# Optimization experiments

Measured on AMD Instinct MI355X. Metric: run time of the kernel, lower is better.

## Reference

```python
import jax, jax.numpy as jnp
import numpy as np

N, T, E = 50000, 8, 800000
X_DIM, H_DIM, Z_DIM = 128, 64, 32


def setup_inputs() -> dict:
    key = jax.random.key(0)
    k = jax.random.split(key, 6)
    x = jax.random.normal(k[0], (N, X_DIM), dtype=jnp.float32)
    ei = jax.random.randint(k[1], (T, 2, E), 0, N, dtype=jnp.int32)
    ew = jax.random.uniform(k[2], (T, E), dtype=jnp.float32)
    W1 = jax.random.normal(k[3], (X_DIM, H_DIM), dtype=jnp.float32) * 0.1
    b1 = jnp.zeros((H_DIM,), dtype=jnp.float32)
    W2 = jax.random.normal(k[4], (H_DIM, Z_DIM), dtype=jnp.float32) * 0.1
    b2 = jnp.zeros((Z_DIM,), dtype=jnp.float32)
    return {"x": x, "ei": ei, "ew": ew, "W1": W1, "b1": b1, "W2": W2, "b2": b2}


def gcn_layer(x, src, dst, ew, W, b):
    # PyG GCNConv with add_self_loops=True (self-loop weight 1):
    #   out = D^{-1/2} (A + I) D^{-1/2} (x @ W) + b,  deg from edge weights at dst
    n = x.shape[0]
    loop = jnp.arange(n, dtype=src.dtype)
    s = jnp.concatenate([src, loop])            # [E+N]
    d = jnp.concatenate([dst, loop])            # [E+N]
    w = jnp.concatenate([ew, jnp.ones((n,), ew.dtype)])
    deg = jax.ops.segment_sum(w, d, num_segments=n)      # [N]
    dinv = jnp.where(deg > 0, jax.lax.rsqrt(deg), 0.0)
    norm = dinv[s] * w * dinv[d]                # [E+N]
    h = x @ W                                    # [N, out_dim] linear first
    out = jax.ops.segment_sum(h[s] * norm[:, None], d, num_segments=n)
    return out + b


def reference(x, ei, ew, W1, b1, W2, b2):
    # eval mode: Dropout(0.25) and DropEdge(0.5) are identity (inner_forward calls self.eval())
    def step(carry, inputs):
        ei_t, ew_t = inputs
        src, dst = ei_t[0], ei_t[1]
        h = jax.nn.relu(gcn_layer(x, src, dst, ew_t, W1, b1))
        z = jnp.tanh(gcn_layer(h, src, dst, ew_t, W2, b2))
        return carry, z
    _, zs = jax.lax.scan(step, None, (ei, ew))   # [T, N, Z_DIM]
    return zs
```

## Files before the change

kernel.cpp:

```cpp
#include <hip/hip_runtime.h>
#include <hip/hip_fp16.h>
#include <math.h>

#define N_NODES 50000
#define T_STEPS 8
#define E_EDGES 800000
#define XD 128
#define HD 64
#define ZD 32
#define M_TOT (T_STEPS * N_NODES)
#define TE_TOT (T_STEPS * E_EDGES)

#define NBKT 196
#define BPT 125
#define EPB 6400
#define NBLK_A (T_STEPS * BPT)
#define CNTA_LEN (T_STEPS * NBKT * BPT)
#define NBUCK_T (T_STEPS * NBKT)
#define BKT_CAP 4864

#define SCAN_CH 2048
#define SCANA_NB ((CNTA_LEN + SCAN_CH - 1) / SCAN_CH)

__device__ __forceinline__ float4 h4tof4(ushort4 u) {
  return make_float4(__half2float(__ushort_as_half(u.x)),
                     __half2float(__ushort_as_half(u.y)),
                     __half2float(__ushort_as_half(u.z)),
                     __half2float(__ushort_as_half(u.w)));
}
__device__ __forceinline__ float cnorm(unsigned int c) {
  return __half2float(__ushort_as_half((unsigned short)(c >> 16)));
}

__global__ __launch_bounds__(256) void k_h0(const float* __restrict__ x,
                                            const float* __restrict__ W1,
                                            unsigned short* __restrict__ h0h) {
  __shared__ float xs[256 * 33];
  __shared__ float w1s[32 * 64];
  const int tid = threadIdx.x;
  const int nb = blockIdx.x * 256;
  const int nl_base = tid & 63;
  const int jg = tid >> 6;
  const float4* x4 = (const float4*)x;
  const float4* W14 = (const float4*)W1;

  float acc[4][16];
#pragma unroll
  for (int i = 0; i < 4; ++i)
#pragma unroll
    for (int j = 0; j < 16; ++j) acc[i][j] = 0.f;

  for (int kc = 0; kc < 4; ++kc) {
#pragma unroll
    for (int r = 0; r < 8; ++r) {
      int f4 = tid + r * 256;
      int nl = f4 >> 3;
      int k4 = f4 & 7;
      float4 v = make_float4(0.f, 0.f, 0.f, 0.f);
      int node = nb + nl;
      if (node < N_NODES) v = x4[node * 32 + kc * 8 + k4];
      int base = nl * 33 + k4 * 4;
      xs[base + 0] = v.x; xs[base + 1] = v.y;
      xs[base + 2] = v.z; xs[base + 3] = v.w;
    }
#pragma unroll
    for (int r = 0; r < 2; ++r) {
      int f4 = tid + r * 256;
      ((float4*)w1s)[f4] = W14[kc * 512 + f4];
    }
    __syncthreads();
#pragma unroll 4
    for (int k = 0; k < 32; ++k) {
      float xv[4];
#pragma unroll
      for (int i = 0; i < 4; ++i) xv[i] = xs[(nl_base + i * 64) * 33 + k];
      const float* wr = &w1s[k * 64 + jg * 16];
      float4 w0 = *(const float4*)(wr + 0);
      float4 w1v = *(const float4*)(wr + 4);
      float4 w2v = *(const float4*)(wr + 8);
      float4 w3v = *(const float4*)(wr + 12);
#pragma unroll
      for (int i = 0; i < 4; ++i) {
        acc[i][0] += xv[i] * w0.x;  acc[i][1] += xv[i] * w0.y;
        acc[i][2] += xv[i] * w0.z;  acc[i][3] += xv[i] * w0.w;
        acc[i][4] += xv[i] * w1v.x; acc[i][5] += xv[i] * w1v.y;
        acc[i][6] += xv[i] * w1v.z; acc[i][7] += xv[i] * w1v.w;
        acc[i][8] += xv[i] * w2v.x; acc[i][9] += xv[i] * w2v.y;
        acc[i][10] += xv[i] * w2v.z; acc[i][11] += xv[i] * w2v.w;
        acc[i][12] += xv[i] * w3v.x; acc[i][13] += xv[i] * w3v.y;
        acc[i][14] += xv[i] * w3v.z; acc[i][15] += xv[i] * w3v.w;
      }
    }
    __syncthreads();
  }
  ushort4* h4p = (ushort4*)h0h;
#pragma unroll
  for (int i = 0; i < 4; ++i) {
    int node = nb + nl_base + i * 64;
    if (node < N_NODES) {
#pragma unroll
      for (int q = 0; q < 4; ++q) {
        ushort4 s;
        s.x = __half_as_ushort(__float2half(acc[i][q * 4 + 0]));
        s.y = __half_as_ushort(__float2half(acc[i][q * 4 + 1]));
        s.z = __half_as_ushort(__float2half(acc[i][q * 4 + 2]));
        s.w = __half_as_ushort(__float2half(acc[i][q * 4 + 3]));
        h4p[(size_t)node * 16 + jg * 4 + q] = s;
      }
    }
  }
}

__global__ __launch_bounds__(256) void k_binhist(const int* __restrict__ ei,
                                                 unsigned short* __restrict__ rankA,
                                                 unsigned int* __restrict__ cntA) {
  __shared__ unsigned int hist[NBKT];
  const int tid = threadIdx.x, bid = blockIdx.x;
  const int t = bid / BPT, b = bid - t * BPT;
  if (tid < NBKT) hist[tid] = 0;
  __syncthreads();
  const int* dstp = ei + (t * 2 + 1) * E_EDGES + b * EPB;
  const int gbase = t * E_EDGES + b * EPB;
#pragma unroll
  for (int it = 0; it < EPB / 256; ++it) {
    int e = it * 256 + tid;
    int dst = dstp[e];
    unsigned int r = atomicAdd(&hist[dst >> 8], 1u);
    rankA[gbase + e] = (unsigned short)r;
  }
  __syncthreads();
  if (tid < NBKT) cntA[(t * NBKT + tid) * BPT + b] = hist[tid];
}

__global__ __launch_bounds__(256) void k_scan1(const unsigned int* __restrict__ cntA,
                                               int* __restrict__ bsum) {
  __shared__ int s[256];
  int bid = blockIdx.x, tid = threadIdx.x;
  int base = bid * SCAN_CH;
  int v = 0;
#pragma unroll
  for (int r = 0; r < 8; ++r) {
    int i = base + tid + r * 256;
    if (i < CNTA_LEN) v += (int)cntA[i];
  }
  s[tid] = v;
  __syncthreads();
  for (int off = 128; off > 0; off >>= 1) {
    if (tid < off) s[tid] += s[tid + off];
    __syncthreads();
  }
  if (tid == 0) bsum[bid] = s[0];
}

__global__ __launch_bounds__(256) void k_scan2(const int* __restrict__ bsum,
                                               int* __restrict__ bpre) {
  __shared__ int s[256];
  int tid = threadIdx.x;
  int v = (tid < SCANA_NB) ? bsum[tid] : 0;
  s[tid] = v;
  __syncthreads();
  for (int off = 1; off < 256; off <<= 1) {
    int t = (tid >= off) ? s[tid - off] : 0;
    __syncthreads();
    s[tid] += t;
    __syncthreads();
  }
  bpre[tid] = s[tid] - v;
}

__global__ __launch_bounds__(256) void k_scan3(const unsigned int* __restrict__ cntA,
                                               const int* __restrict__ bpre,
                                               unsigned int* __restrict__ scannedA) {
  __shared__ int s[256];
  int bid = blockIdx.x, tid = threadIdx.x;
  int i0 = bid * SCAN_CH + tid * 8;
  int c[8];
  int lsum = 0;
#pragma unroll
  for (int j = 0; j < 8; ++j) {
    int i = i0 + j;
    c[j] = (i < CNTA_LEN) ? (int)cntA[i] : 0;
    lsum += c[j];
  }
  int v = lsum;
  s[tid] = v;
  __syncthreads();
  for (int off = 1; off < 256; off <<= 1) {
    int t = (tid >= off) ? s[tid - off] : 0;
    __syncthreads();
    s[tid] += t;
    __syncthreads();
  }
  int run = bpre[bid] + (s[tid] - v);
#pragma unroll
  for (int j = 0; j < 8; ++j) {
    int i = i0 + j;
    if (i < CNTA_LEN) {
      scannedA[i] = (unsigned int)run;
      run += c[j];
    }
  }
}

__global__ __launch_bounds__(256) void k_binscatter(const int* __restrict__ ei,
                                                    const float* __restrict__ ew,
                                                    const unsigned short* __restrict__ rankA,
                                                    const unsigned int* __restrict__ scannedA,
                                                    uint2* __restrict__ ebuf) {
  int i = blockIdx.x * 256 + threadIdx.x;
  int t = i / E_EDGES;
  int e = i - t * E_EDGES;
  int b = e / EPB;
  int src = ei[t * 2 * E_EDGES + e];
  int dst = ei[(t * 2 + 1) * E_EDGES + e];
  float w = ew[i];
  int bkt = dst >> 8;
  unsigned int pos = scannedA[(t * NBKT + bkt) * BPT + b] + rankA[i];
  ebuf[pos] = make_uint2(((unsigned int)(dst & 255) << 16) | (unsigned int)src,
                         __float_as_uint(w));
}

__global__ __launch_bounds__(256) void k_bucket1(const uint2* __restrict__ ebuf,
                                                 const unsigned int* __restrict__ scannedA,
                                                 unsigned int* __restrict__ localscan,
                                                 float* __restrict__ dinv,
                                                 int* __restrict__ row_off) {
  __shared__ unsigned int cnt[256];
  __shared__ float degs[256];
  __shared__ unsigned int sc[256];
  const int tid = threadIdx.x, blk = blockIdx.x;
  const int t = blk / NBKT, bkt = blk - t * NBKT;
  const unsigned int base = scannedA[blk * BPT];
  const unsigned int end = (blk == NBUCK_T - 1) ? (unsigned int)TE_TOT
                                                : scannedA[(blk + 1) * BPT];
  cnt[tid] = 0;
  degs[tid] = 0.f;
  __syncthreads();
  for (unsigned int i = base + tid; i < end; i += 256) {
    uint2 v = ebuf[i];
    unsigned int dlo = v.x >> 16;
    atomicAdd(&cnt[dlo], 1u);
    atomicAdd(&degs[dlo], __uint_as_float(v.y));
  }
  __syncthreads();
  unsigned int myc = cnt[tid];
  sc[tid] = myc;
  __syncthreads();
  for (int off = 1; off < 256; off <<= 1) {
    unsigned int a = (tid >= off) ? sc[tid - off] : 0;
    __syncthreads();
    sc[tid] += a;
    __syncthreads();
  }
  unsigned int start = base + (sc[tid] - myc);
  localscan[blk * 256 + tid] = start;
  int dst = bkt * 256 + tid;
  if (dst < N_NODES) {
    int tn = t * N_NODES + dst;
    dinv[tn] = rsqrtf(1.0f + degs[tid]);
    row_off[tn] = (int)start;
  }
  if (blk == NBUCK_T - 1 && tid == 0) row_off[M_TOT] = TE_TOT;
}

__global__ __launch_bounds__(256) void k_bucket2(const uint2* __restrict__ ebuf,
                                                 const unsigned int* __restrict__ scannedA,
                                                 const unsigned int* __restrict__ localscan,
                                                 const float* __restrict__ dinv,
                                                 unsigned int* __restrict__ csr32) {
  __shared__ uint2 stage[BKT_CAP];
  __shared__ unsigned int cursor[256];
  const int tid = threadIdx.x, blk = blockIdx.x;
  const int t = blk / NBKT;
  const unsigned int base = scannedA[blk * BPT];
  const unsigned int end = (blk == NBUCK_T - 1) ? (unsigned int)TE_TOT
                                                : scannedA[(blk + 1) * BPT];
  cursor[tid] = localscan[blk * 256 + tid];
  const unsigned int n = end - base;
  for (unsigned int j = tid; j < n; j += 256) stage[j] = ebuf[base + j];
  __syncthreads();
  const float* dv = dinv + t * N_NODES;
  for (unsigned int j = tid; j < n; j += 256) {
    uint2 v = stage[j];
    unsigned int dlo = v.x >> 16;
    unsigned int src = v.x & 0xFFFFu;
    unsigned int slot = atomicAdd(&cursor[dlo], 1u);
    float norm = __uint_as_float(v.y) * dv[src];
    csr32[slot] = src | ((unsigned int)__half_as_ushort(__float2half(norm)) << 16);
  }
}

__global__ __launch_bounds__(256) void k_gather1(
    const unsigned short* __restrict__ h0h, const float* __restrict__ dinv,
    const int* __restrict__ row_off, const unsigned int* __restrict__ csr,
    const float* __restrict__ W2, const float* __restrict__ b1,
    unsigned short* __restrict__ g16) {
  __shared__ float h1s[16 * 65];
  __shared__ float w2s[64 * 32];
  const int tid = threadIdx.x;
#pragma unroll
  for (int r = 0; r < 2; ++r)
    ((float4*)w2s)[tid + r * 256] = ((const float4*)W2)[tid + r * 256];

  const int grp = tid >> 4;
  const int lane = tid & 15;
  const int tn = blockIdx.x * 16 + grp;
  const int t = tn / N_NODES;
  const int n = tn - t * N_NODES;
  const float dvn = dinv[tn];
  const ushort4* h4 = (const ushort4*)h0h;
  float4 bv = ((const float4*)b1)[lane];

  float4 acc = h4tof4(h4[(size_t)n * 16 + lane]);
  acc.x *= dvn; acc.y *= dvn; acc.z *= dvn; acc.w *= dvn;

  const int e0 = row_off[tn], e1 = row_off[tn + 1];
  int e = e0;
  for (; e + 4 <= e1; e += 4) {
    unsigned int c0 = csr[e + 0], c1 = csr[e + 1];
    unsigned int c2 = csr[e + 2], c3 = csr[e + 3];
    ushort4 u0 = h4[(size_t)(c0 & 0xFFFFu) * 16 + lane];
    ushort4 u1 = h4[(size_t)(c1 & 0xFFFFu) * 16 + lane];
    ushort4 u2 = h4[(size_t)(c2 & 0xFFFFu) * 16 + lane];
    ushort4 u3 = h4[(size_t)(c3 & 0xFFFFu) * 16 + lane];
    float n0 = cnorm(c0), n1 = cnorm(c1), n2 = cnorm(c2), n3 = cnorm(c3);
    float4 f0 = h4tof4(u0), f1 = h4tof4(u1), f2 = h4tof4(u2), f3 = h4tof4(u3);
    acc.x += n0 * f0.x + n1 * f1.x + n2 * f2.x + n3 * f3.x;
    acc.y += n0 * f0.y + n1 * f1.y + n2 * f2.y + n3 * f3.y;
    acc.z += n0 * f0.z + n1 * f1.z + n2 * f2.z + n3 * f3.z;
    acc.w += n0 * f0.w + n1 * f1.w + n2 * f2.w + n3 * f3.w;
  }
  for (; e < e1; ++e) {
    unsigned int c = csr[e];
    ushort4 u = h4[(size_t)(c & 0xFFFFu) * 16 + lane];
    float nn = cnorm(c);
    float4 f = h4tof4(u);
    acc.x += nn * f.x; acc.y += nn * f.y;
    acc.z += nn * f.z; acc.w += nn * f.w;
  }
  int hb = grp * 65 + lane * 4;
  h1s[hb + 0] = fmaxf(acc.x * dvn + bv.x, 0.f);
  h1s[hb + 1] = fmaxf(acc.y * dvn + bv.y, 0.f);
  h1s[hb + 2] = fmaxf(acc.z * dvn + bv.z, 0.f);
  h1s[hb + 3] = fmaxf(acc.w * dvn + bv.w, 0.f);
  __syncthreads();

  const int n1i = tid >> 5;
  const int j = tid & 31;
  float a0 = 0.f, a1 = 0.f;
#pragma unroll 8
  for (int k = 0; k < 64; ++k) {
    float wv = w2s[k * 32 + j];
    a0 += h1s[n1i * 65 + k] * wv;
    a1 += h1s[(n1i + 8) * 65 + k] * wv;
  }
  const int tnb = blockIdx.x * 16;
  g16[(size_t)(tnb + n1i) * 32 + j] = __half_as_ushort(__float2half(a0));
  g16[(size_t)(tnb + n1i + 8) * 32 + j] = __half_as_ushort(__float2half(a1));
}

__global__ __launch_bounds__(256) void k_gather2(
    const unsigned short* __restrict__ g16, const float* __restrict__ dinv,
    const int* __restrict__ row_off, const unsigned int* __restrict__ csr,
    const float* __restrict__ b2, float* __restrict__ out) {
  const int nwg = gridDim.x;
  const int orig = blockIdx.x;
  const int xcd = orig & 7, lid = orig >> 3;
  const int q = nwg >> 3, r = nwg & 7;
  const int bid = (xcd < r ? xcd * (q + 1) : r * (q + 1) + (xcd - r) * q) + lid;

  const int tid = threadIdx.x;
  const int grp = tid >> 3;
  const int lane = tid & 7;
  const int tn = bid * 32 + grp;
  const int t = tn / N_NODES;
  const int tbase = t * N_NODES;
  const float dvn = dinv[tn];
  const ushort4* g4 = (const ushort4*)g16;
  float4 bv = ((const float4*)b2)[lane];

  float4 acc = h4tof4(g4[(size_t)tn * 8 + lane]);
  acc.x *= dvn; acc.y *= dvn; acc.z *= dvn; acc.w *= dvn;

  const int e0 = row_off[tn], e1 = row_off[tn + 1];
  int e = e0;
  for (; e + 4 <= e1; e += 4) {
    unsigned int c0 = csr[e + 0], c1 = csr[e + 1];
    unsigned int c2 = csr[e + 2], c3 = csr[e + 3];
    ushort4 u0 = g4[(size_t)(tbase + (int)(c0 & 0xFFFFu)) * 8 + lane];
    ushort4 u1 = g4[(size_t)(tbase + (int)(c1 & 0xFFFFu)) * 8 + lane];
    ushort4 u2 = g4[(size_t)(tbase + (int)(c2 & 0xFFFFu)) * 8 + lane];
    ushort4 u3 = g4[(size_t)(tbase + (int)(c3 & 0xFFFFu)) * 8 + lane];
    float n0 = cnorm(c0), n1 = cnorm(c1), n2 = cnorm(c2), n3 = cnorm(c3);
    float4 f0 = h4tof4(u0), f1 = h4tof4(u1), f2 = h4tof4(u2), f3 = h4tof4(u3);
    acc.x += n0 * f0.x + n1 * f1.x + n2 * f2.x + n3 * f3.x;
    acc.y += n0 * f0.y + n1 * f1.y + n2 * f2.y + n3 * f3.y;
    acc.z += n0 * f0.z + n1 * f1.z + n2 * f2.z + n3 * f3.z;
    acc.w += n0 * f0.w + n1 * f1.w + n2 * f2.w + n3 * f3.w;
  }
  for (; e < e1; ++e) {
    unsigned int c = csr[e];
    ushort4 u = g4[(size_t)(tbase + (int)(c & 0xFFFFu)) * 8 + lane];
    float nn = cnorm(c);
    float4 f = h4tof4(u);
    acc.x += nn * f.x; acc.y += nn * f.y;
    acc.z += nn * f.z; acc.w += nn * f.w;
  }
  float4 z;
  z.x = tanhf(acc.x * dvn + bv.x);
  z.y = tanhf(acc.y * dvn + bv.y);
  z.z = tanhf(acc.z * dvn + bv.z);
  z.w = tanhf(acc.w * dvn + bv.w);
  ((float4*)out)[(size_t)tn * 8 + lane] = z;
}

extern "C" void kernel_launch(void* const* d_in, const int* in_sizes, int n_in,
                              void* d_out, int out_size, void* d_ws, size_t ws_size,
                              hipStream_t stream) {
  const float* x = (const float*)d_in[0];
  const int* ei = (const int*)d_in[1];
  const float* ew = (const float*)d_in[2];
  const float* W1 = (const float*)d_in[3];
  const float* b1 = (const float*)d_in[4];
  const float* W2 = (const float*)d_in[5];
  const float* b2 = (const float*)d_in[6];
  float* out = (float*)d_out;

  char* base = (char*)d_ws;
  size_t o = 0;
  auto alloc = [&](size_t bytes) -> char* {
    char* r = base + o;
    o = (o + bytes + 255) & ~(size_t)255;
    return r;
  };
  unsigned short* h0h = (unsigned short*)alloc((size_t)N_NODES * HD * 2);
  float* dinv = (float*)alloc((size_t)M_TOT * 4);
  int* row_off = (int*)alloc((size_t)(M_TOT + 1) * 4);
  unsigned int* localscan = (unsigned int*)alloc((size_t)NBUCK_T * 256 * 4);
  unsigned int* cntA = (unsigned int*)alloc((size_t)CNTA_LEN * 4);
  unsigned int* scannedA = (unsigned int*)alloc((size_t)CNTA_LEN * 4);
  int* bsum = (int*)alloc(1024);
  int* bpre = (int*)alloc(1024);
  uint2* ebuf = (uint2*)alloc((size_t)TE_TOT * 8);
  unsigned int* csr32 = (unsigned int*)alloc((size_t)TE_TOT * 4);
  unsigned short* g16 = (unsigned short*)alloc((size_t)M_TOT * ZD * 2);
  unsigned short* rankA = (unsigned short*)g16;

  k_h0<<<(N_NODES + 255) / 256, 256, 0, stream>>>(x, W1, h0h);
  k_binhist<<<NBLK_A, 256, 0, stream>>>(ei, rankA, cntA);
  k_scan1<<<SCANA_NB, 256, 0, stream>>>(cntA, bsum);
  k_scan2<<<1, 256, 0, stream>>>(bsum, bpre);
  k_scan3<<<SCANA_NB, 256, 0, stream>>>(cntA, bpre, scannedA);
  k_binscatter<<<TE_TOT / 256, 256, 0, stream>>>(ei, ew, rankA, scannedA, ebuf);
  k_bucket1<<<NBUCK_T, 256, 0, stream>>>(ebuf, scannedA, localscan, dinv, row_off);
  k_bucket2<<<NBUCK_T, 256, 0, stream>>>(ebuf, scannedA, localscan, dinv, csr32);
  k_gather1<<<M_TOT / 16, 256, 0, stream>>>(h0h, dinv, row_off, csr32, W2, b1, g16);
  k_gather2<<<M_TOT / 32, 256, 0, stream>>>(g16, dinv, row_off, csr32, b2, out);
}
```

Measured before the change: 590.7 us.

## Software-pipeline gather loops with branchless quads and drop bucket LDS staging

Both gather kernels now run a double-buffered loop: the next quad of CSR entries and neighbour rows is loaded before the current quad is accumulated. Tail handling is done with clamped indices and zeroed weights, and 32-bit index arithmetic replaces 64-bit. k_bucket2 no longer stages the bucket's edges in shared memory and reads them straight from global memory, which lowers LDS use and may raise occupancy. Workspace buffers are reordered, and the padded tail lanes issue extra redundant loads.

```diff
diff --git a/kernel.cpp b/kernel.cpp
--- a/kernel.cpp
+++ b/kernel.cpp
@@ -17,7 +17,6 @@
 #define NBLK_A (T_STEPS * BPT)
 #define CNTA_LEN (T_STEPS * NBKT * BPT)
 #define NBUCK_T (T_STEPS * NBKT)
-#define BKT_CAP 4864
 
 #define SCAN_CH 2048
 #define SCANA_NB ((CNTA_LEN + SCAN_CH - 1) / SCAN_CH)
@@ -268,7 +267,6 @@
                                                  const unsigned int* __restrict__ localscan,
                                                  const float* __restrict__ dinv,
                                                  unsigned int* __restrict__ csr32) {
-  __shared__ uint2 stage[BKT_CAP];
   __shared__ unsigned int cursor[256];
   const int tid = threadIdx.x, blk = blockIdx.x;
   const int t = blk / NBKT;
@@ -276,12 +274,10 @@
   const unsigned int end = (blk == NBUCK_T - 1) ? (unsigned int)TE_TOT
                                                 : scannedA[(blk + 1) * BPT];
   cursor[tid] = localscan[blk * 256 + tid];
-  const unsigned int n = end - base;
-  for (unsigned int j = tid; j < n; j += 256) stage[j] = ebuf[base + j];
   __syncthreads();
   const float* dv = dinv + t * N_NODES;
-  for (unsigned int j = tid; j < n; j += 256) {
-    uint2 v = stage[j];
+  for (unsigned int i = base + tid; i < end; i += 256) {
+    uint2 v = ebuf[i];
     unsigned int dlo = v.x >> 16;
     unsigned int src = v.x & 0xFFFFu;
     unsigned int slot = atomicAdd(&cursor[dlo], 1u);
@@ -303,7 +299,7 @@
     ((float4*)w2s)[tid + r * 256] = ((const float4*)W2)[tid + r * 256];
 
   const int grp = tid >> 4;
-  const int lane = tid & 15;
+  const unsigned lane = tid & 15;
   const int tn = blockIdx.x * 16 + grp;
   const int t = tn / N_NODES;
   const int n = tn - t * N_NODES;
@@ -311,34 +307,46 @@
   const ushort4* h4 = (const ushort4*)h0h;
   float4 bv = ((const float4*)b1)[lane];
 
-  float4 acc = h4tof4(h4[(size_t)n * 16 + lane]);
+  float4 acc = h4tof4(h4[(unsigned)n * 16u + lane]);
   acc.x *= dvn; acc.y *= dvn; acc.z *= dvn; acc.w *= dvn;
 
   const int e0 = row_off[tn], e1 = row_off[tn + 1];
-  int e = e0;
-  for (; e + 4 <= e1; e += 4) {
-    unsigned int c0 = csr[e + 0], c1 = csr[e + 1];
-    unsigned int c2 = csr[e + 2], c3 = csr[e + 3];
-    ushort4 u0 = h4[(size_t)(c0 & 0xFFFFu) * 16 + lane];
-    ushort4 u1 = h4[(size_t)(c1 & 0xFFFFu) * 16 + lane];
-    ushort4 u2 = h4[(size_t)(c2 & 0xFFFFu) * 16 + lane];
-    ushort4 u3 = h4[(size_t)(c3 & 0xFFFFu) * 16 + lane];
-    float n0 = cnorm(c0), n1 = cnorm(c1), n2 = cnorm(c2), n3 = cnorm(c3);
-    float4 f0 = h4tof4(u0), f1 = h4tof4(u1), f2 = h4tof4(u2), f3 = h4tof4(u3);
-    acc.x += n0 * f0.x + n1 * f1.x + n2 * f2.x + n3 * f3.x;
-    acc.y += n0 * f0.y + n1 * f1.y + n2 * f2.y + n3 * f3.y;
-    acc.z += n0 * f0.z + n1 * f1.z + n2 * f2.z + n3 * f3.z;
-    acc.w += n0 * f0.w + n1 * f1.w + n2 * f2.w + n3 * f3.w;
-  }
-  for (; e < e1; ++e) {
-    unsigned int c = csr[e];
-    ushort4 u = h4[(size_t)(c & 0xFFFFu) * 16 + lane];
-    float nn = cnorm(c);
-    float4 f = h4tof4(u);
-    acc.x += nn * f.x; acc.y += nn * f.y;
-    acc.z += nn * f.z; acc.w += nn * f.w;
-  }
-  int hb = grp * 65 + lane * 4;
+  const int e1m1 = e1 - 1;
+  const int nq = (e1 - e0 + 3) >> 2;
+
+  float nA[4], nB[4];
+  ushort4 uA[4], uB[4];
+
+#define LOADQ1(qe, nn, uu)                                        \
+  {                                                               \
+    _Pragma("unroll") for (int k_ = 0; k_ < 4; ++k_) {            \
+      int ee = (qe) + k_;                                         \
+      unsigned cc = csr[ee < e1m1 ? ee : e1m1];                   \
+      nn[k_] = (ee < e1) ? cnorm(cc) : 0.f;                       \
+      uu[k_] = h4[(cc & 0xFFFFu) * 16u + lane];                   \
+    }                                                             \
+  }
+#define FMAQ1(nn, uu)                                             \
+  {                                                               \
+    _Pragma("unroll") for (int k_ = 0; k_ < 4; ++k_) {            \
+      float4 f = h4tof4(uu[k_]);                                  \
+      acc.x += nn[k_] * f.x; acc.y += nn[k_] * f.y;               \
+      acc.z += nn[k_] * f.z; acc.w += nn[k_] * f.w;               \
+    }                                                             \
+  }
+
+  int q = 0;
+  if (nq > 0) LOADQ1(e0, nA, uA);
+  while (q + 2 <= nq) {
+    LOADQ1(e0 + (q + 1) * 4, nB, uB);
+    FMAQ1(nA, uA);
+    if (q + 3 <= nq) LOADQ1(e0 + (q + 2) * 4, nA, uA);
+    FMAQ1(nB, uB);
+    q += 2;
+  }
+  if (q < nq) FMAQ1(nA, uA);
+
+  int hb = grp * 65 + (int)lane * 4;
   h1s[hb + 0] = fmaxf(acc.x * dvn + bv.x, 0.f);
   h1s[hb + 1] = fmaxf(acc.y * dvn + bv.y, 0.f);
   h1s[hb + 2] = fmaxf(acc.z * dvn + bv.z, 0.f);
@@ -366,46 +374,50 @@
   const int nwg = gridDim.x;
   const int orig = blockIdx.x;
   const int xcd = orig & 7, lid = orig >> 3;
-  const int q = nwg >> 3, r = nwg & 7;
-  const int bid = (xcd < r ? xcd * (q + 1) : r * (q + 1) + (xcd - r) * q) + lid;
+  const int qq = nwg >> 3, rr = nwg & 7;
+  const int bid = (xcd < rr ? xcd * (qq + 1) : rr * (qq + 1) + (xcd - rr) * qq) + lid;
 
   const int tid = threadIdx.x;
   const int grp = tid >> 3;
-  const int lane = tid & 7;
+  const unsigned lane = tid & 7;
   const int tn = bid * 32 + grp;
   const int t = tn / N_NODES;
-  const int tbase = t * N_NODES;
+  const unsigned tbase = (unsigned)(t * N_NODES);
   const float dvn = dinv[tn];
   const ushort4* g4 = (const ushort4*)g16;
   float4 bv = ((const float4*)b2)[lane];
 
-  float4 acc = h4tof4(g4[(size_t)tn * 8 + lane]);
+  float4 acc = h4tof4(g4[(unsigned)tn * 8u + lane]);
   acc.x *= dvn; acc.y *= dvn; acc.z *= dvn; acc.w *= dvn;
 
   const int e0 = row_off[tn], e1 = row_off[tn + 1];
-  int e = e0;
-  for (; e + 4 <= e1; e += 4) {
-    unsigned int c0 = csr[e + 0], c1 = csr[e + 1];
-    unsigned int c2 = csr[e + 2], c3 = csr[e + 3];
-    ushort4 u0 = g4[(size_t)(tbase + (int)(c0 & 0xFFFFu)) * 8 + lane];
-    ushort4 u1 = g4[(size_t)(tbase + (int)(c1 & 0xFFFFu)) * 8 + lane];
-    ushort4 u2 = g4[(size_t)(tbase + (int)(c2 & 0xFFFFu)) * 8 + lane];
-    ushort4 u3 = g4[(size_t)(tbase + (int)(c3 & 0xFFFFu)) * 8 + lane];
-    float n0 = cnorm(c0), n1 = cnorm(c1), n2 = cnorm(c2), n3 = cnorm(c3);
-    float4 f0 = h4tof4(u0), f1 = h4tof4(u1), f2 = h4tof4(u2), f3 = h4tof4(u3);
-    acc.x += n0 * f0.x + n1 * f1.x + n2 * f2.x + n3 * f3.x;
-    acc.y += n0 * f0.y + n1 * f1.y + n2 * f2.y + n3 * f3.y;
-    acc.z += n0 * f0.z + n1 * f1.z + n2 * f2.z + n3 * f3.z;
-    acc.w += n0 * f0.w + n1 * f1.w + n2 * f2.w + n3 * f3.w;
-  }
-  for (; e < e1; ++e) {
-    unsigned int c = csr[e];
-    ushort4 u = g4[(size_t)(tbase + (int)(c & 0xFFFFu)) * 8 + lane];
-    float nn = cnorm(c);
-    float4 f = h4tof4(u);
-    acc.x += nn * f.x; acc.y += nn * f.y;
-    acc.z += nn * f.z; acc.w += nn * f.w;
-  }
+  const int e1m1 = e1 - 1;
+  const int nq = (e1 - e0 + 3) >> 2;
+
+  float nA[4], nB[4];
+  ushort4 uA[4], uB[4];
+
+#define LOADQ2(qe, nn, uu)                                        \
+  {                                                               \
+    _Pragma("unroll") for (int k_ = 0; k_ < 4; ++k_) {            \
+      int ee = (qe) + k_;                                         \
+      unsigned cc = csr[ee < e1m1 ? ee : e1m1];                   \
+      nn[k_] = (ee < e1) ? cnorm(cc) : 0.f;                       \
+      uu[k_] = g4[(tbase + (cc & 0xFFFFu)) * 8u + lane];          \
+    }                                                             \
+  }
+
+  int q = 0;
+  if (nq > 0) LOADQ2(e0, nA, uA);
+  while (q + 2 <= nq) {
+    LOADQ2(e0 + (q + 1) * 4, nB, uB);
+    FMAQ1(nA, uA);
+    if (q + 3 <= nq) LOADQ2(e0 + (q + 2) * 4, nA, uA);
+    FMAQ1(nB, uB);
+    q += 2;
+  }
+  if (q < nq) FMAQ1(nA, uA);
+
   float4 z;
   z.x = tanhf(acc.x * dvn + bv.x);
   z.y = tanhf(acc.y * dvn + bv.y);
@@ -441,9 +453,9 @@
   unsigned int* scannedA = (unsigned int*)alloc((size_t)CNTA_LEN * 4);
   int* bsum = (int*)alloc(1024);
   int* bpre = (int*)alloc(1024);
+  unsigned short* g16 = (unsigned short*)alloc((size_t)M_TOT * ZD * 2);
+  unsigned int* csr32 = (unsigned int*)alloc((size_t)TE_TOT * 4);
   uint2* ebuf = (uint2*)alloc((size_t)TE_TOT * 8);
-  unsigned int* csr32 = (unsigned int*)alloc((size_t)TE_TOT * 4);
-  unsigned short* g16 = (unsigned short*)alloc((size_t)M_TOT * ZD * 2);
   unsigned short* rankA = (unsigned short*)g16;
 
   k_h0<<<(N_NODES + 255) / 256, 256, 0, stream>>>(x, W1, h0h);
```

New measurement: 595.8 us. No clear change (+0.9%).
